# Performance work log

Measured on AMD Instinct MI355X. Metric: run time of the kernel, lower is better.

The kernel has to match this reference:

```python
import jax, jax.numpy as jnp
import numpy as np

B, S, HID = 1, 2048, 1024
HQ, HKV, D = 16, 8, 64
W = 64          # causal window size (includes self at offset 0)
K = 128         # total neighbors per query: W window + (K-W) random rewires


def setup_inputs() -> dict:
    key = jax.random.key(0)
    ks = jax.random.split(key, 8)
    hidden_states = jax.random.normal(ks[0], (B, S, HID), jnp.float32)
    sc = HID ** -0.5
    q_w = jax.random.normal(ks[1], (HQ * D, HID), jnp.float32) * sc
    k_w = jax.random.normal(ks[2], (HKV * D, HID), jnp.float32) * sc
    v_w = jax.random.normal(ks[3], (HKV * D, HID), jnp.float32) * sc
    o_w = jax.random.normal(ks[4], (HQ * D, HID), jnp.float32).T * sc  # [HID, HQ*D] -> stored as [HID, HQ*D]? keep [HID, HQ*D]
    o_w = jax.random.normal(ks[4], (HID, HQ * D), jnp.float32) * sc
    edge_bias = jax.random.normal(ks[5], (4,), jnp.float32) * 0.1
    # neighbor indices: per kv-head, per query position.
    pos = jnp.arange(S)
    win = pos[:, None] - jnp.arange(W)[None, :]                    # [S, W], offset 0 == self
    win = jnp.broadcast_to(win[None], (HKV, S, W))
    rew = jax.random.randint(ks[6], (HKV, S, K - W), 0, S)         # random rewire edges
    neigh_idx = jnp.concatenate([win, rew], axis=-1).astype(jnp.int32)  # [HKV, S, K]
    edge_type = jnp.concatenate([
        jnp.full((HKV, S, W), 1, jnp.int32),       # 'window'
        jnp.full((HKV, S, K - W), 3, jnp.int32),   # 'rewire'
    ], axis=-1)
    return {
        'hidden_states': hidden_states, 'q_w': q_w, 'k_w': k_w, 'v_w': v_w,
        'o_w': o_w, 'edge_bias': edge_bias, 'neigh_idx': neigh_idx,
        'edge_type': edge_type,
    }


def reference(hidden_states, q_w, k_w, v_w, o_w, edge_bias, neigh_idx, edge_type):
    b, s, _ = hidden_states.shape
    hkv, _, kk = neigh_idx.shape
    hq = q_w.shape[0] // (k_w.shape[0] // hkv)
    d = k_w.shape[0] // hkv
    hq = q_w.shape[0] // d
    g = hq // hkv
    scaling = d ** -0.5

    # projections (nn.Linear: x @ W.T)
    q = (hidden_states @ q_w.T).reshape(b, s, hq, d).transpose(0, 2, 1, 3)    # [B,HQ,S,D]
    k = (hidden_states @ k_w.T).reshape(b, s, hkv, d).transpose(0, 2, 1, 3)   # [B,HKV,S,D]
    v = (hidden_states @ v_w.T).reshape(b, s, hkv, d).transpose(0, 2, 1, 3)

    # causal neighbor mask + safe clamp (mirrors _causal_neighbor_mask / _safe_neighbor_idx)
    pos = jnp.arange(s)
    mask = (neigh_idx >= 0) & (neigh_idx < s) & (neigh_idx <= pos[None, :, None])  # [HKV,S,K]
    safe = jnp.clip(neigh_idx, 0, s - 1)

    # gather K/V at neighbor indices: [B,HKV,S,K,D]
    h_idx = jnp.arange(hkv)[:, None, None]
    k_g = k[:, h_idx, safe, :]
    v_g = v[:, h_idx, safe, :]

    # GQA: group query heads over kv heads
    qg = q.reshape(b, hkv, g, s, d)
    scores = jnp.einsum('bhgsd,bhskd->bhgsk', qg, k_g) * scaling              # [B,HKV,G,S,K]
    scores = scores + edge_bias[edge_type][None, :, None, :, :]
    neg = jnp.finfo(scores.dtype).min
    scores = jnp.where(mask[None, :, None, :, :], scores, neg)
    attn = jax.nn.softmax(scores, axis=-1)

    out = jnp.einsum('bhgsk,bhskd->bhgsd', attn, v_g)                         # [B,HKV,G,S,D]
    out = out.reshape(b, hq, s, d).transpose(0, 2, 1, 3).reshape(b, s, hq * d)
    return out @ o_w.T                                                        # [B,S,HID]
```

## Files before the change

kernel.cpp:

```cpp
#include <hip/hip_runtime.h>
#include <hip/hip_bf16.h>

#define S_LEN 2048
#define HIDDEN 1024

typedef __attribute__((ext_vector_type(4))) float f32x4;
typedef __attribute__((ext_vector_type(8))) _Float16 f16x8;
typedef __attribute__((ext_vector_type(2))) _Float16 f16x2;
typedef __attribute__((ext_vector_type(2))) __fp16 fp16x2;
typedef unsigned short u16;
typedef unsigned int u32;

typedef const __attribute__((address_space(1))) unsigned int as1_u32;
typedef __attribute__((address_space(3))) unsigned int as3_u32;

__device__ __forceinline__ u16 f2h(float f) {
  union { _Float16 h; u16 u; } c; c.h = (_Float16)f; return c.u;
}
__device__ __forceinline__ f16x2 u2h2(u32 u) {
  union { u32 x; f16x2 h; } c; c.x = u; return c.h;
}
__device__ __forceinline__ float fdot2(u32 a, u32 b, float c) {
#if __has_builtin(__builtin_amdgcn_fdot2)
  return __builtin_amdgcn_fdot2(u2h2(a), u2h2(b), c, false);
#else
  f16x2 ha = u2h2(a), hb = u2h2(b);
  return fmaf((float)ha.x, (float)hb.x, fmaf((float)ha.y, (float)hb.y, c));
#endif
}
__device__ __forceinline__ u32 pkrtz(float a, float b) {
#if __has_builtin(__builtin_amdgcn_cvt_pkrtz)
  union { fp16x2 h; u32 u; } c;
  c.h = __builtin_amdgcn_cvt_pkrtz(a, b);
  return c.u;
#else
  union { f16x2 h; u32 u; } c;
  c.h.x = (_Float16)a; c.h.y = (_Float16)b;
  return c.u;
#endif
}

__global__ __launch_bounds__(256) void cvt_all(
    const float* __restrict__ h, const float* __restrict__ qw,
    const float* __restrict__ kw, const float* __restrict__ vw,
    const float* __restrict__ ow, u16* __restrict__ hb, u16* __restrict__ qwb,
    u16* __restrict__ kwb, u16* __restrict__ vwb, u16* __restrict__ owb) {
  const int b = blockIdx.x;
  const float* src; u16* dst; int base;
  if (b < 2048)      { src = h;  dst = hb;  base = b; }
  else if (b < 3072) { src = qw; dst = qwb; base = b - 2048; }
  else if (b < 3584) { src = kw; dst = kwb; base = b - 3072; }
  else if (b < 4096) { src = vw; dst = vwb; base = b - 3584; }
  else               { src = ow; dst = owb; base = b - 4096; }
  const int i = base * 256 + threadIdx.x;
  const float4 v = ((const float4*)src)[i];
  ushort4 r;
  r.x = f2h(v.x); r.y = f2h(v.y); r.z = f2h(v.z); r.w = f2h(v.w);
  ((ushort4*)dst)[i] = r;
}

template <int BM, bool OUT_F16>
__device__ __forceinline__ void gemm_core(
    u16* __restrict__ As, u16* __restrict__ Bs,
    const u16* __restrict__ A, const u16* __restrict__ W, void* __restrict__ Cv,
    int Kd, int ldc, int mtile, int ntile) {
  constexpr int MF = BM / 32;
  const int tid = threadIdx.x;
  const int lane = tid & 63;
  const int wave = tid >> 6;
  const int wr = wave >> 1, wc = wave & 1;
  f32x4 acc[MF][4] = {};
  const int m0 = mtile * BM, n0 = ntile * 128;

  for (int kt = 0; kt < Kd; kt += 32) {
#pragma unroll
    for (int i = 0; i < BM / 64; ++i) {
      const int e = (i * 256 + tid) * 8;
      const int r = e >> 5, c = e & 31;
      __builtin_amdgcn_global_load_lds(
          (as1_u32*)(A + (size_t)(m0 + r) * Kd + kt + c), (as3_u32*)(As + e), 16, 0, 0);
    }
#pragma unroll
    for (int i = 0; i < 2; ++i) {
      const int e = (i * 256 + tid) * 8;
      const int r = e >> 5, c = e & 31;
      __builtin_amdgcn_global_load_lds(
          (as1_u32*)(W + (size_t)(n0 + r) * Kd + kt + c), (as3_u32*)(Bs + e), 16, 0, 0);
    }
    __syncthreads();
    f16x8 af[MF], bfr[4];
#pragma unroll
    for (int mi = 0; mi < MF; ++mi)
      af[mi] = *(const f16x8*)(As + (wr * (BM / 2) + mi * 16 + (lane & 15)) * 32 + (lane >> 4) * 8);
#pragma unroll
    for (int ni = 0; ni < 4; ++ni)
      bfr[ni] = *(const f16x8*)(Bs + (wc * 64 + ni * 16 + (lane & 15)) * 32 + (lane >> 4) * 8);
#pragma unroll
    for (int mi = 0; mi < MF; ++mi)
#pragma unroll
      for (int ni = 0; ni < 4; ++ni)
        acc[mi][ni] = __builtin_amdgcn_mfma_f32_16x16x32_f16(af[mi], bfr[ni], acc[mi][ni], 0, 0, 0);
    __syncthreads();
  }

#pragma unroll
  for (int mi = 0; mi < MF; ++mi) {
#pragma unroll
    for (int ni = 0; ni < 4; ++ni) {
      const int row0 = m0 + wr * (BM / 2) + mi * 16 + (lane >> 4) * 4;
      const int col = n0 + wc * 64 + ni * 16 + (lane & 15);
#pragma unroll
      for (int r = 0; r < 4; ++r) {
        if (OUT_F16)
          ((u16*)Cv)[(size_t)(row0 + r) * ldc + col] = f2h(acc[mi][ni][r]);
        else
          ((float*)Cv)[(size_t)(row0 + r) * ldc + col] = acc[mi][ni][r];
      }
    }
  }
}

__global__ __launch_bounds__(256, 2) void qkv_gemm(
    const u16* __restrict__ hb, const u16* __restrict__ qwb,
    const u16* __restrict__ kwb, const u16* __restrict__ vwb,
    u16* __restrict__ Qb, u16* __restrict__ Kb, u16* __restrict__ Vb) {
  __shared__ u16 As[128 * 32];
  __shared__ u16 Bs[128 * 32];
  const int nt = blockIdx.x, mt = blockIdx.y;
  if (nt < 8)       gemm_core<128, true>(As, Bs, hb, qwb, Qb, HIDDEN, 1024, mt, nt);
  else if (nt < 12) gemm_core<128, true>(As, Bs, hb, kwb, Kb, HIDDEN, 512, mt, nt - 8);
  else              gemm_core<128, true>(As, Bs, hb, vwb, Vb, HIDDEN, 512, mt, nt - 12);
}

__global__ __launch_bounds__(256, 2) void o_gemm(
    const u16* __restrict__ attnb, const u16* __restrict__ owb,
    float* __restrict__ out) {
  __shared__ u16 As[64 * 32];
  __shared__ u16 Bs[128 * 32];
  gemm_core<64, false>(As, Bs, attnb, owb, out, HIDDEN, 1024, blockIdx.y, blockIdx.x);
}

#define WIN_ROWS 72
#define WIN_ELEMS (WIN_ROWS * 64)
__global__ __launch_bounds__(512, 2) void attn_kernel(
    const u16* __restrict__ Qb, const u16* __restrict__ Kb,
    const u16* __restrict__ Vb, const int* __restrict__ neigh,
    const float* __restrict__ ebias, u16* __restrict__ attnb) {
  __shared__ u16 smem[WIN_ELEMS + 8 * 4096];

  const int tid = threadIdx.x;
  const int lane = tid & 63;
  const int wv = tid >> 6;
  const int h = blockIdx.y;
  const int s0 = blockIdx.x * 8;
  const int s = s0 + wv;

  const u16* Kp = Kb + h * 64;
  const u16* Vp = Vb + h * 64;

  const int iB = neigh[((size_t)h * S_LEN + s) * 128 + 64 + lane];
  const bool okB = (iB >= 0) && (iB <= s);
  const int gB = min(max(iB, 0), S_LEN - 1);
  const bool okA = lane <= s;

  u16* kwin = smem;
  u16* krw = smem + WIN_ELEMS + wv * 4096;
  const int chunk = (lane & 7) ^ (lane >> 3);

  {
    int g = wv;
    int r_lds = g * 8 + (lane >> 3);
    int row = min(max(s0 - 63 + r_lds, 0), S_LEN - 1);
    __builtin_amdgcn_global_load_lds(
        (as1_u32*)(Kp + (size_t)row * 512 + chunk * 8),
        (as3_u32*)(kwin + g * 512 + lane * 8), 16, 0, 0);
    if (wv == 0) {
      g = 8;
      r_lds = g * 8 + (lane >> 3);
      row = min(max(s0 - 63 + r_lds, 0), S_LEN - 1);
      __builtin_amdgcn_global_load_lds(
          (as1_u32*)(Kp + (size_t)row * 512 + chunk * 8),
          (as3_u32*)(kwin + g * 512 + lane * 8), 16, 0, 0);
    }
  }
#pragma unroll
  for (int g2 = 0; g2 < 8; ++g2) {
    const int row = __shfl(gB, g2 * 8 + (lane >> 3));
    __builtin_amdgcn_global_load_lds(
        (as1_u32*)(Kp + (size_t)row * 512 + chunk * 8),
        (as3_u32*)(krw + g2 * 512 + lane * 8), 16, 0, 0);
  }

  __syncthreads();

  const u16* qp = Qb + (size_t)s * 1024 + h * 128;
  const int rW = wv + 63 - lane;
  const u16* kwrow = kwin + rW * 64;
  const u16* krrow = krw + lane * 64;
  const int rw7 = rW & 7, ln7 = lane & 7;
  float sA0 = 0.f, sA1 = 0.f, sB0 = 0.f, sB1 = 0.f;
#pragma unroll
  for (int t = 0; t < 8; ++t) {
    const uint4 kw = *(const uint4*)(kwrow + ((t ^ rw7) << 3));
    const uint4 kr = *(const uint4*)(krrow + ((t ^ ln7) << 3));
    const uint4 qa = *(const uint4*)(qp + t * 8);
    const uint4 qb = *(const uint4*)(qp + 64 + t * 8);
    sA0 = fdot2(kw.x, qa.x, sA0); sA0 = fdot2(kw.y, qa.y, sA0);
    sA0 = fdot2(kw.z, qa.z, sA0); sA0 = fdot2(kw.w, qa.w, sA0);
    sA1 = fdot2(kw.x, qb.x, sA1); sA1 = fdot2(kw.y, qb.y, sA1);
    sA1 = fdot2(kw.z, qb.z, sA1); sA1 = fdot2(kw.w, qb.w, sA1);
    sB0 = fdot2(kr.x, qa.x, sB0); sB0 = fdot2(kr.y, qa.y, sB0);
    sB0 = fdot2(kr.z, qa.z, sB0); sB0 = fdot2(kr.w, qa.w, sB0);
    sB1 = fdot2(kr.x, qb.x, sB1); sB1 = fdot2(kr.y, qb.y, sB1);
    sB1 = fdot2(kr.z, qb.z, sB1); sB1 = fdot2(kr.w, qb.w, sB1);
  }

  const float NEG = -1e30f;
  const float SC = 0.125f;
  const float ebW = ebias[1];
  const float ebR = ebias[3];
  sA0 = okA ? fmaf(sA0, SC, ebW) : NEG;
  sA1 = okA ? fmaf(sA1, SC, ebW) : NEG;
  sB0 = okB ? fmaf(sB0, SC, ebR) : NEG;
  sB1 = okB ? fmaf(sB1, SC, ebR) : NEG;

  float m0 = fmaxf(sA0, sB0), m1 = fmaxf(sA1, sB1);
#pragma unroll
  for (int off = 32; off; off >>= 1) {
    m0 = fmaxf(m0, __shfl_xor(m0, off));
    m1 = fmaxf(m1, __shfl_xor(m1, off));
  }
  float eA0 = __expf(sA0 - m0), eB0 = __expf(sB0 - m0);
  float eA1 = __expf(sA1 - m1), eB1 = __expf(sB1 - m1);
  float d0 = eA0 + eB0, d1 = eA1 + eB1;
#pragma unroll
  for (int off = 32; off; off >>= 1) {
    d0 += __shfl_xor(d0, off);
    d1 += __shfl_xor(d1, off);
  }
  const float rc0 = 1.0f / d0, rc1 = 1.0f / d1;

  asm volatile("s_waitcnt lgkmcnt(0)" ::: "memory");
  u32* pb = (u32*)krw;
  int* ib = (int*)(krw + 512);
  const float pA0 = eA0 * rc0, pA1 = eA1 * rc1;
  const float pB0 = eB0 * rc0, pB1 = eB1 * rc1;
  const float hA0 = __shfl_xor(pA0, 1), hA1 = __shfl_xor(pA1, 1);
  const float hB0 = __shfl_xor(pB0, 1), hB1 = __shfl_xor(pB1, 1);
  ib[lane] = gB;
  if (!(lane & 1)) {
    uint4 pk;
    pk.x = pkrtz(pA0, hA0);
    pk.y = pkrtz(pA1, hA1);
    pk.z = pkrtz(pB0, hB0);
    pk.w = pkrtz(pB1, hB1);
    *(uint4*)(pb + (lane >> 1) * 4) = pk;
  }
  asm volatile("" ::: "memory");

  float a0 = 0.f, a1 = 0.f;
#pragma unroll 4
  for (int m = 0; m < 32; ++m) {
    const uint4 pp = *(const uint4*)(pb + m * 4);
    const int2 rB = *(const int2*)(ib + m * 2);
    int r0w = s - 2 * m, r1w = r0w - 1;
    r0w = max(r0w, 0); r1w = max(r1w, 0);
    const u32 w0 = Vp[(size_t)r0w * 512 + lane];
    const u32 w1 = Vp[(size_t)r1w * 512 + lane];
    const u32 b0 = Vp[(size_t)rB.x * 512 + lane];
    const u32 b1 = Vp[(size_t)rB.y * 512 + lane];
    const u32 wpair = (w1 << 16) | w0;
    const u32 bpair = (b1 << 16) | b0;
    a0 = fdot2(wpair, pp.x, a0);
    a1 = fdot2(wpair, pp.y, a1);
    a0 = fdot2(bpair, pp.z, a0);
    a1 = fdot2(bpair, pp.w, a1);
  }

  u16* op = attnb + (size_t)s * 1024 + h * 128;
  op[lane] = f2h(a0);
  op[64 + lane] = f2h(a1);
}

extern "C" void kernel_launch(void* const* d_in, const int* in_sizes, int n_in,
                              void* d_out, int out_size, void* d_ws, size_t ws_size,
                              hipStream_t stream) {
  const float* hidden = (const float*)d_in[0];
  const float* q_w = (const float*)d_in[1];
  const float* k_w = (const float*)d_in[2];
  const float* v_w = (const float*)d_in[3];
  const float* o_w = (const float*)d_in[4];
  const float* ebias = (const float*)d_in[5];
  const int* neigh = (const int*)d_in[6];
  float* out = (float*)d_out;

  char* ws = (char*)d_ws;
  u16* hb    = (u16*)(ws + (0ull << 20));
  u16* qwb   = (u16*)(ws + (4ull << 20));
  u16* kwb   = (u16*)(ws + (6ull << 20));
  u16* vwb   = (u16*)(ws + (7ull << 20));
  u16* owb   = (u16*)(ws + (8ull << 20));
  u16* Qb    = (u16*)(ws + (10ull << 20));
  u16* Kb    = (u16*)(ws + (14ull << 20));
  u16* Vb    = (u16*)(ws + (16ull << 20));
  u16* attnb = (u16*)(ws + (18ull << 20));

  cvt_all<<<5120, 256, 0, stream>>>(hidden, q_w, k_w, v_w, o_w,
                                    hb, qwb, kwb, vwb, owb);
  qkv_gemm<<<dim3(16, 16), 256, 0, stream>>>(hb, qwb, kwb, vwb, Qb, Kb, Vb);
  attn_kernel<<<dim3(256, 8), 512, 0, stream>>>(Qb, Kb, Vb, neigh, ebias, attnb);
  o_gemm<<<dim3(8, 32), 256, 0, stream>>>(attnb, owb, out);
}
```

Measured before the change: 94.27 us.

## Shrink attention blocks, stage V window in LDS, load rewire keys to registers

The attention kernel now runs 4 queries per 256-thread block instead of 8 per 512-thread block. Each lane loads its rewire K row straight into registers rather than staging it through per-wave LDS. The causal window of V is staged in LDS alongside the K window, so window V reads hit shared memory instead of global memory. This cuts LDS use per block to allow higher occupancy, but the K/V window is now reloaded with more overlap across the doubled number of blocks.

```diff
diff --git a/kernel.cpp b/kernel.cpp
--- a/kernel.cpp
+++ b/kernel.cpp
@@ -142,17 +142,19 @@
 
 #define WIN_ROWS 72
 #define WIN_ELEMS (WIN_ROWS * 64)
-__global__ __launch_bounds__(512, 2) void attn_kernel(
+__global__ __launch_bounds__(256, 5) void attn_kernel(
     const u16* __restrict__ Qb, const u16* __restrict__ Kb,
     const u16* __restrict__ Vb, const int* __restrict__ neigh,
     const float* __restrict__ ebias, u16* __restrict__ attnb) {
-  __shared__ u16 smem[WIN_ELEMS + 8 * 4096];
+  __shared__ u16 kwin[WIN_ELEMS];
+  __shared__ u16 vwin[WIN_ELEMS];
+  __shared__ u32 park[4][192];
 
   const int tid = threadIdx.x;
   const int lane = tid & 63;
   const int wv = tid >> 6;
   const int h = blockIdx.y;
-  const int s0 = blockIdx.x * 8;
+  const int s0 = blockIdx.x * 4;
   const int s = s0 + wv;
 
   const u16* Kp = Kb + h * 64;
@@ -163,32 +165,34 @@
   const int gB = min(max(iB, 0), S_LEN - 1);
   const bool okA = lane <= s;
 
-  u16* kwin = smem;
-  u16* krw = smem + WIN_ELEMS + wv * 4096;
+  const u16* krp = Kp + (size_t)gB * 512;
+  uint4 krreg[8];
+#pragma unroll
+  for (int t = 0; t < 8; ++t) krreg[t] = *(const uint4*)(krp + t * 8);
+
   const int chunk = (lane & 7) ^ (lane >> 3);
-
-  {
-    int g = wv;
-    int r_lds = g * 8 + (lane >> 3);
-    int row = min(max(s0 - 63 + r_lds, 0), S_LEN - 1);
+#pragma unroll
+  for (int gg = 0; gg < 2; ++gg) {
+    const int g = wv + gg * 4;
+    const int r_lds = g * 8 + (lane >> 3);
+    const int row = min(max(s0 - 63 + r_lds, 0), S_LEN - 1);
     __builtin_amdgcn_global_load_lds(
         (as1_u32*)(Kp + (size_t)row * 512 + chunk * 8),
         (as3_u32*)(kwin + g * 512 + lane * 8), 16, 0, 0);
-    if (wv == 0) {
-      g = 8;
-      r_lds = g * 8 + (lane >> 3);
-      row = min(max(s0 - 63 + r_lds, 0), S_LEN - 1);
-      __builtin_amdgcn_global_load_lds(
-          (as1_u32*)(Kp + (size_t)row * 512 + chunk * 8),
-          (as3_u32*)(kwin + g * 512 + lane * 8), 16, 0, 0);
-    }
-  }
-#pragma unroll
-  for (int g2 = 0; g2 < 8; ++g2) {
-    const int row = __shfl(gB, g2 * 8 + (lane >> 3));
+    __builtin_amdgcn_global_load_lds(
+        (as1_u32*)(Vp + (size_t)row * 512 + chunk * 8),
+        (as3_u32*)(vwin + g * 512 + lane * 8), 16, 0, 0);
+  }
+  if (wv == 0) {
+    const int g = 8;
+    const int r_lds = g * 8 + (lane >> 3);
+    const int row = min(max(s0 - 63 + r_lds, 0), S_LEN - 1);
     __builtin_amdgcn_global_load_lds(
         (as1_u32*)(Kp + (size_t)row * 512 + chunk * 8),
-        (as3_u32*)(krw + g2 * 512 + lane * 8), 16, 0, 0);
+        (as3_u32*)(kwin + g * 512 + lane * 8), 16, 0, 0);
+    __builtin_amdgcn_global_load_lds(
+        (as1_u32*)(Vp + (size_t)row * 512 + chunk * 8),
+        (as3_u32*)(vwin + g * 512 + lane * 8), 16, 0, 0);
   }
 
   __syncthreads();
@@ -196,13 +200,12 @@
   const u16* qp = Qb + (size_t)s * 1024 + h * 128;
   const int rW = wv + 63 - lane;
   const u16* kwrow = kwin + rW * 64;
-  const u16* krrow = krw + lane * 64;
-  const int rw7 = rW & 7, ln7 = lane & 7;
+  const int rw7 = rW & 7;
   float sA0 = 0.f, sA1 = 0.f, sB0 = 0.f, sB1 = 0.f;
 #pragma unroll
   for (int t = 0; t < 8; ++t) {
     const uint4 kw = *(const uint4*)(kwrow + ((t ^ rw7) << 3));
-    const uint4 kr = *(const uint4*)(krrow + ((t ^ ln7) << 3));
+    const uint4 kr = krreg[t];
     const uint4 qa = *(const uint4*)(qp + t * 8);
     const uint4 qb = *(const uint4*)(qp + 64 + t * 8);
     sA0 = fdot2(kw.x, qa.x, sA0); sA0 = fdot2(kw.y, qa.y, sA0);
@@ -240,9 +243,8 @@
   }
   const float rc0 = 1.0f / d0, rc1 = 1.0f / d1;
 
-  asm volatile("s_waitcnt lgkmcnt(0)" ::: "memory");
-  u32* pb = (u32*)krw;
-  int* ib = (int*)(krw + 512);
+  u32* pb = park[wv];
+  int* ib = (int*)(park[wv] + 128);
   const float pA0 = eA0 * rc0, pA1 = eA1 * rc1;
   const float pB0 = eB0 * rc0, pB1 = eB1 * rc1;
   const float hA0 = __shfl_xor(pA0, 1), hA1 = __shfl_xor(pA1, 1);
@@ -256,17 +258,20 @@
     pk.w = pkrtz(pB1, hB1);
     *(uint4*)(pb + (lane >> 1) * 4) = pk;
   }
-  asm volatile("" ::: "memory");
+  asm volatile("s_waitcnt lgkmcnt(0)" ::: "memory");
 
   float a0 = 0.f, a1 = 0.f;
+  const int ln7 = lane & 7, lnc = lane >> 3;
 #pragma unroll 4
   for (int m = 0; m < 32; ++m) {
     const uint4 pp = *(const uint4*)(pb + m * 4);
     const int2 rB = *(const int2*)(ib + m * 2);
-    int r0w = s - 2 * m, r1w = r0w - 1;
-    r0w = max(r0w, 0); r1w = max(r1w, 0);
-    const u32 w0 = Vp[(size_t)r0w * 512 + lane];
-    const u32 w1 = Vp[(size_t)r1w * 512 + lane];
+    const int rl0 = wv + 63 - 2 * m;
+    const int rl1 = rl0 - 1;
+    const int a0i = (rl0 >> 3) * 512 + ((rl0 & 7) * 8 + (lnc ^ (rl0 & 7))) * 8 + ln7;
+    const int a1i = (rl1 >> 3) * 512 + ((rl1 & 7) * 8 + (lnc ^ (rl1 & 7))) * 8 + ln7;
+    const u32 w0 = vwin[a0i];
+    const u32 w1 = vwin[a1i];
     const u32 b0 = Vp[(size_t)rB.x * 512 + lane];
     const u32 b1 = Vp[(size_t)rB.y * 512 + lane];
     const u32 wpair = (w1 << 16) | w0;
@@ -308,6 +313,6 @@
   cvt_all<<<5120, 256, 0, stream>>>(hidden, q_w, k_w, v_w, o_w,
                                     hb, qwb, kwb, vwb, owb);
   qkv_gemm<<<dim3(16, 16), 256, 0, stream>>>(hb, qwb, kwb, vwb, Qb, Kb, Vb);
-  attn_kernel<<<dim3(256, 8), 512, 0, stream>>>(Qb, Kb, Vb, neigh, ebias, attnb);
+  attn_kernel<<<dim3(512, 8), 256, 0, stream>>>(Qb, Kb, Vb, neigh, ebias, attnb);
   o_gemm<<<dim3(8, 32), 256, 0, stream>>>(attnb, owb, out);
 }
```

Measured after the change: 95.21 us. About the same (+1.0%).
